# Performance work log

Hardware: AMD Instinct MI355X
Metric: run time of the kernel (lower is better)

Reference implementation:

```python
import jax, jax.numpy as jnp
import numpy as np

D_MODEL = 1024
N_HEADS = 16
HEAD_DIM = D_MODEL // N_HEADS


def _rotary_tables(seq_len, dim):
    # sin/cos tables: (seq_len, dim//2)
    pos = jnp.arange(seq_len, dtype=jnp.float32)[:, None]
    freqs = 1.0 / 10000.0 ** (jnp.arange(0, dim, 2, dtype=jnp.float32) / dim)
    angles = pos * freqs
    return jnp.sin(angles), jnp.cos(angles)


def _apply_rotary(x, sin, cos):
    # x: (B, H, N, head_dim); sin/cos: (N, head_dim//2) broadcast over B,H
    d_half = x.shape[-1] // 2
    x1, x2 = x[..., :d_half], x[..., d_half:]
    return jnp.concatenate([x1 * cos - x2 * sin, x1 * sin + x2 * cos], axis=-1)


def setup_inputs() -> dict:
    key = jax.random.key(0)
    k_x, k_q, k_k, k_v, k_o = jax.random.split(key, 5)
    B, N = 4, 2048
    scale = 1.0 / np.sqrt(D_MODEL)
    return {
        "x": jax.random.normal(k_x, (B, N, D_MODEL), dtype=jnp.float32),
        "Wq": jax.random.normal(k_q, (D_MODEL, D_MODEL), dtype=jnp.float32) * scale,
        "Wk": jax.random.normal(k_k, (D_MODEL, D_MODEL), dtype=jnp.float32) * scale,
        "Wv": jax.random.normal(k_v, (D_MODEL, D_MODEL), dtype=jnp.float32) * scale,
        "Wo": jax.random.normal(k_o, (D_MODEL, D_MODEL), dtype=jnp.float32) * scale,
    }


def reference(x, Wq, Wk, Wv, Wo):
    B, N, _ = x.shape
    # nn.Linear(d, d, bias=False): y = x @ W.T ; view+transpose -> (B, H, N, hd)
    def proj(W):
        return jnp.einsum('bnd,ed->bne', x, W).reshape(B, N, N_HEADS, HEAD_DIM).transpose(0, 2, 1, 3)

    Q, K, V = proj(Wq), proj(Wk), proj(Wv)
    sin, cos = _rotary_tables(N, HEAD_DIM)
    Q = _apply_rotary(Q, sin, cos)
    K = _apply_rotary(K, sin, cos)

    # SDPA (non-causal, dropout=0): softmax(Q K^T / sqrt(hd)) V
    scores = jnp.einsum('bhqd,bhkd->bhqk', Q, K) / jnp.sqrt(jnp.asarray(HEAD_DIM, x.dtype))
    attn = jax.nn.softmax(scores, axis=-1)
    out = jnp.einsum('bhqk,bhkd->bhqd', attn, V)  # (B, H, N, hd)
    out = out.transpose(0, 2, 1, 3).reshape(B, N, D_MODEL)
    return jnp.einsum('bnd,ed->bne', out, Wo)
```

## Files before the change

kernel.cpp:

```cpp
#include <hip/hip_runtime.h>
#include <stdint.h>

#define SEQ    2048
#define DMODEL 1024
#define NHEADS 16
#define HDIM   64
#define BATCH  4
#define MTOT   (BATCH*SEQ)

typedef __attribute__((ext_vector_type(8)))  short s16x8;
typedef __attribute__((ext_vector_type(4)))  short s16x4;
typedef __attribute__((ext_vector_type(4)))  float f32x4;
typedef __attribute__((ext_vector_type(16))) float f32x16;

#define OFF_SIN  ((size_t)0)
#define OFF_COS  ((size_t)262144)
#define OFF_XHI  ((size_t)524288)
#define OFF_WQH  ((size_t)34078720)
#define OFF_WKH  ((size_t)38273024)
#define OFF_WVH  ((size_t)42467328)
#define OFF_WOH  ((size_t)46661632)
#define OFF_QR   ((size_t)50855936)
#define OFF_KR   ((size_t)67633152)
#define OFF_VT   ((size_t)84410368)
#define OFF_AHI  ((size_t)101187584)

#define QSCALE 0.18033688011112042f

__device__ __forceinline__ uint16_t f2bf(float f){
  union{float f;uint32_t u;}v; v.f=f;
  uint32_t r=v.u+0x7fffu+((v.u>>16)&1u);
  return (uint16_t)(r>>16);
}
__device__ __forceinline__ float bf2f(uint16_t u){
  union{uint32_t u;float f;}v; v.u=((uint32_t)u)<<16; return v.f;
}

__device__ __forceinline__ void async16(void* lds, const void* g){
  __builtin_amdgcn_global_load_lds(
    (const __attribute__((address_space(1))) void*)g,
    (__attribute__((address_space(3))) void*)lds, 16, 0, 0);
}

__device__ __forceinline__ float fexp2(float x){
#if __has_builtin(__builtin_amdgcn_exp2f)
  return __builtin_amdgcn_exp2f(x);
#else
  float r; asm("v_exp_f32 %0, %1" : "=v"(r) : "v"(x)); return r;
#endif
}
__device__ __forceinline__ float frcp(float x){
#if __has_builtin(__builtin_amdgcn_rcpf)
  return __builtin_amdgcn_rcpf(x);
#else
  float r; asm("v_rcp_f32 %0, %1" : "=v"(r) : "v"(x)); return r;
#endif
}
__device__ __forceinline__ void plswap(unsigned a, unsigned b, unsigned &o0, unsigned &o1){
#if __has_builtin(__builtin_amdgcn_permlane32_swap)
  auto r = __builtin_amdgcn_permlane32_swap(a, b, false, false);
  o0 = (unsigned)r[0]; o1 = (unsigned)r[1];
#else
  unsigned ax = (unsigned)__shfl_xor((int)a, 32, 64);
  unsigned bx = (unsigned)__shfl_xor((int)b, 32, 64);
  bool hi = (threadIdx.x & 32) != 0;
  o0 = hi ? bx : a;
  o1 = hi ? b  : ax;
#endif
}

__global__ __launch_bounds__(256) void prep_k(
  const float* __restrict__ x,
  const float* __restrict__ Wq, const float* __restrict__ Wk,
  const float* __restrict__ Wv, const float* __restrict__ Wo,
  uint16_t* __restrict__ xhi, uint16_t* __restrict__ wqh, uint16_t* __restrict__ wkh,
  uint16_t* __restrict__ wvh, uint16_t* __restrict__ woh,
  float* __restrict__ st, float* __restrict__ ct)
{
  int b = blockIdx.x;
  if (b < 12288){
    const float* s; uint16_t* d; int i;
    if (b < 8192){ s = x; d = xhi; i = b*256 + threadIdx.x; }
    else {
      int wsel = (b - 8192) >> 10;
      int lb   = (b - 8192) & 1023;
      s = wsel==0? Wq : wsel==1? Wk : wsel==2? Wv : Wo;
      d = wsel==0? wqh: wsel==1? wkh: wsel==2? wvh: woh;
      i = lb*256 + threadIdx.x;
    }
    f32x4 v = *(const f32x4*)(s + (size_t)i*4);
    s16x4 vh;
    #pragma unroll
    for(int r=0;r<4;r++) vh[r] = (short)f2bf(v[r]);
    *(s16x4*)(d + (size_t)i*4) = vh;
  } else {
    int i = (b - 12288)*256 + threadIdx.x;
    int n = i>>5, j = i&31;
    double freq = pow(10000.0, -(double)j/32.0);
    double ang = (double)n*freq;
    st[i] = (float)sin(ang);
    ct[i] = (float)cos(ang);
  }
}

__device__ __forceinline__ void gemm_mainloop64(
  const uint16_t* __restrict__ A, const uint16_t* __restrict__ B,
  int m0, int e0, char* lA, char* lB, f32x4 acc[4][4])
{
  const int t = threadIdx.x;
  const int lane = t & 63;
  const int wr = t>>7, wc = (t>>6)&1;
  const int lq = lane&15, lg = lane>>4;
  const int rowA = wr*64 + lq;
  const int rowB = wc*64 + lq;

  int dbyte[4], srow[4], sbyte[4];
  #pragma unroll
  for (int s=0;s<4;s++){
    int d = s*4096 + t*16;
    int r = d>>7, c = (d>>4)&7;
    dbyte[s]=d; srow[s]=r; sbyte[s]=(c ^ (r&7))*16;
  }
  int chh[2];
  #pragma unroll
  for (int kh=0;kh<2;kh++) chh[kh] = (((kh<<2)|lg) ^ (lq&7))*16;

  const char* Ab = (const char*)A;
  const char* Bb = (const char*)B;

  for (int k0=0; k0<DMODEL; k0+=64){
    #pragma unroll
    for (int s=0;s<4;s++){
      async16(lA + dbyte[s], Ab + (size_t)(m0+srow[s])*2048 + k0*2 + sbyte[s]);
      async16(lB + dbyte[s], Bb + (size_t)(e0+srow[s])*2048 + k0*2 + sbyte[s]);
    }
    __syncthreads();
    #pragma unroll
    for (int kh=0;kh<2;kh++){
      s16x8 af[4], bfr[4];
      #pragma unroll
      for (int mi=0;mi<4;mi++) af[mi]  = *(const s16x8*)(lA + (rowA+mi*16)*128 + chh[kh]);
      #pragma unroll
      for (int ni=0;ni<4;ni++) bfr[ni] = *(const s16x8*)(lB + (rowB+ni*16)*128 + chh[kh]);
      __builtin_amdgcn_s_setprio(1);
      #pragma unroll
      for (int mi=0;mi<4;mi++){
        #pragma unroll
        for (int ni=0;ni<4;ni++)
          acc[mi][ni] = __builtin_amdgcn_mfma_f32_16x16x32_bf16(af[mi], bfr[ni], acc[mi][ni],0,0,0);
      }
      __builtin_amdgcn_s_setprio(0);
    }
    __syncthreads();
  }
}

__global__ __launch_bounds__(256) void gemm_qkv_k(
  const uint16_t* __restrict__ Xh,
  const uint16_t* __restrict__ WqH, const uint16_t* __restrict__ WkH, const uint16_t* __restrict__ WvH,
  const float* __restrict__ st, const float* __restrict__ ct,
  uint16_t* __restrict__ Qr, uint16_t* __restrict__ Kr, uint16_t* __restrict__ Vt)
{
  __shared__ char lA[128*128], lB[128*128];
  int m0 = blockIdx.x*128;
  int cti = blockIdx.y;
  int seg = cti>>3;
  int e0 = (cti&7)*128;
  const uint16_t* W = seg==0? WqH : (seg==1? WkH : WvH);
  f32x4 acc[4][4];
  #pragma unroll
  for(int i=0;i<4;i++){
    #pragma unroll
    for(int j=0;j<4;j++) acc[i][j] = (f32x4){0.f,0.f,0.f,0.f};
  }
  gemm_mainloop64(Xh, W, m0, e0, lA, lB, acc);

  int t=threadIdx.x, lane=t&63, lq=lane&15, lg=lane>>4;
  int wr=t>>7, wc=(t>>6)&1;
  int eb = e0 + wc*64;
  int h = eb>>6;
  int rbase = m0 + wr*64 + lg*4;
  if (seg<2){
    uint16_t* O = seg==0? Qr:Kr;
    float qs = seg==0 ? QSCALE : 1.0f;
    #pragma unroll
    for(int mi=0;mi<4;mi++){
      #pragma unroll
      for(int ni=0;ni<2;ni++){
        int j = ni*16+lq;
        #pragma unroll
        for(int r=0;r<4;r++){
          int m = rbase + mi*16 + r;
          int b = m>>11, n = m&2047;
          float sv = st[n*32+j], cv = ct[n*32+j];
          float x1 = acc[mi][ni][r], x2 = acc[mi][ni+2][r];
          size_t base = ((size_t)((b*NHEADS+h)*SEQ + n))*HDIM;
          O[base + j]      = f2bf((x1*cv - x2*sv)*qs);
          O[base + j + 32] = f2bf((x1*sv + x2*cv)*qs);
        }
      }
    }
  } else {
    #pragma unroll
    for(int mi=0;mi<4;mi++){
      #pragma unroll
      for(int ni=0;ni<4;ni++){
        int dh = ni*16+lq;
        int m = rbase + mi*16;
        int b = m>>11, n = m&2047;
        s16x4 v;
        #pragma unroll
        for(int r=0;r<4;r++) v[r] = (short)f2bf(acc[mi][ni][r]);
        *(s16x4*)(Vt + ((size_t)((b*NHEADS+h)*HDIM + dh))*SEQ + n) = v;
      }
    }
  }
}

__global__ __launch_bounds__(256) void attn_k(
  const uint16_t* __restrict__ Qr, const uint16_t* __restrict__ Kr, const uint16_t* __restrict__ Vt,
  uint16_t* __restrict__ Ah)
{
  __shared__ char lds[32768];

  int bid = blockIdx.x;
  int w = (bid & 7)*128 + (bid >> 3);
  int bh = w >> 4, qt = w & 15;
  int tid = threadIdx.x;
  int wid = tid >> 6, lane = tid & 63;
  int l31 = lane & 31, hi = lane >> 5;
  int q0 = qt*128 + wid*32;

  const uint16_t* Qb = Qr + (size_t)bh*SEQ*HDIM;
  const uint16_t* Kb = Kr + (size_t)bh*SEQ*HDIM;
  const uint16_t* Vb = Vt + (size_t)bh*HDIM*SEQ;

  s16x8 qf[4];
  #pragma unroll
  for (int sp=0; sp<4; ++sp)
    qf[sp] = *(const s16x8*)(Qb + (size_t)(q0 + l31)*HDIM + sp*16 + hi*8);

  s16x8 ones;
  #pragma unroll
  for (int j=0;j<8;j++) ones[j] = (short)0x3F80;

  f32x16 zm16;
  #pragma unroll
  for (int r=0;r<16;r++) zm16[r] = -16.0f;

  f32x16 oa[2], lacc;
  #pragma unroll
  for (int r=0;r<16;r++){ oa[0][r]=0.f; oa[1][r]=0.f; lacc[r]=0.f; }

  const int e7 = l31 & 7;
  const int rK = l31*128;
  const int kOff[4]  = { (((0+hi)^e7)<<4), (((2+hi)^e7)<<4), (((4+hi)^e7)<<4), (((6+hi)^e7)<<4) };
  const int vA0 = (((0+hi)^e7)<<4), vA1 = (((2+hi)^e7)<<4);
  const int vB0 = (((4+hi)^e7)<<4), vB1 = (((6+hi)^e7)<<4);
  const bool odd = (wid & 1) != 0;
  const int kBaseF = odd ? 4096 : 0,   kBaseS = odd ? 0 : 4096;
  const int vF0 = odd ? vB0 : vA0,     vF1 = odd ? vB1 : vA1;
  const int vS0 = odd ? vA0 : vB0,     vS1 = odd ? vA1 : vB1;

  auto STAGE = [&](int buf, int t){
    const char* Ks = (const char*)(Kb + (size_t)t*64*HDIM);
    char* dK = lds + buf*8192;
    char* dV = lds + 16384 + buf*8192;
    #pragma unroll
    for (int r=0; r<2; ++r){
      int ci = r*256 + tid;
      int sc = ci ^ ((ci>>3)&7);
      async16(dK + ci*16, Ks + sc*16);
    }
    #pragma unroll
    for (int r=0; r<2; ++r){
      int ci = r*256 + tid;
      int row = ci>>3;
      int sc = (ci&7) ^ (row&7);
      async16(dV + ci*16, (const char*)Vb + ((size_t)row*SEQ + (size_t)t*64)*2 + sc*16);
    }
  };

  auto SUBSTEP = [&](const char* bK, const char* bV, int kbase, int v0, int v1){
    s16x8 kf[4];
    #pragma unroll
    for (int sp=0; sp<4; ++sp)
      kf[sp] = *(const s16x8*)(bK + kbase + rK + kOff[sp]);
    f32x16 sacc = zm16;
    __builtin_amdgcn_s_setprio(1);
    #pragma unroll
    for (int sp=0; sp<4; ++sp)
      sacc = __builtin_amdgcn_mfma_f32_32x32x16_bf16(kf[sp], qf[sp], sacc, 0,0,0);
    __builtin_amdgcn_s_setprio(0);
    s16x8 vf[4];
    #pragma unroll
    for (int db=0; db<2; ++db){
      vf[db*2+0] = *(const s16x8*)(bV + db*4096 + rK + v0);
      vf[db*2+1] = *(const s16x8*)(bV + db*4096 + rK + v1);
    }
    float p[16];
    #pragma unroll
    for (int r=0;r<16;r++) p[r] = fexp2(sacc[r]);
    uint32_t pw[8];
    #pragma unroll
    for (int j=0;j<8;j++)
      asm("v_cvt_pk_bf16_f32 %0, %1, %2" : "=v"(pw[j]) : "v"(p[2*j]), "v"(p[2*j+1]));
    unsigned w0,w1,w2,w3, x0,x1,x2,x3;
    plswap(pw[0], pw[2], w0, w2);
    plswap(pw[1], pw[3], w1, w3);
    plswap(pw[4], pw[6], x0, x2);
    plswap(pw[5], pw[7], x1, x3);
    union { uint32_t wd[4]; s16x8 v; } pa0, pa1;
    pa0.wd[0]=w0; pa0.wd[1]=w1; pa0.wd[2]=w2; pa0.wd[3]=w3;
    pa1.wd[0]=x0; pa1.wd[1]=x1; pa1.wd[2]=x2; pa1.wd[3]=x3;
    __builtin_amdgcn_s_setprio(1);
    oa[0] = __builtin_amdgcn_mfma_f32_32x32x16_bf16(pa0.v, vf[0], oa[0], 0,0,0);
    oa[0] = __builtin_amdgcn_mfma_f32_32x32x16_bf16(pa1.v, vf[1], oa[0], 0,0,0);
    oa[1] = __builtin_amdgcn_mfma_f32_32x32x16_bf16(pa0.v, vf[2], oa[1], 0,0,0);
    oa[1] = __builtin_amdgcn_mfma_f32_32x32x16_bf16(pa1.v, vf[3], oa[1], 0,0,0);
    lacc = __builtin_amdgcn_mfma_f32_32x32x16_bf16(pa0.v, ones, lacc, 0,0,0);
    lacc = __builtin_amdgcn_mfma_f32_32x32x16_bf16(pa1.v, ones, lacc, 0,0,0);
    __builtin_amdgcn_s_setprio(0);
  };

  STAGE(0, 0);
  asm volatile("s_waitcnt vmcnt(0)" ::: "memory");
  __syncthreads();

  const int NT = SEQ/64;
  for (int t=0; t<NT; ++t){
    int cur = t & 1;
    if (t+1 < NT) STAGE(cur^1, t+1);
    const char* bK = lds + cur*8192;
    const char* bV = lds + 16384 + cur*8192;
    SUBSTEP(bK, bV, kBaseF, vF0, vF1);
    SUBSTEP(bK, bV, kBaseS, vS0, vS1);
    asm volatile("s_waitcnt vmcnt(0)" ::: "memory");
    __syncthreads();
  }

  int b = bh >> 4, h = bh & 15;
  #pragma unroll
  for (int r=0;r<16;r++){
    int q = (r&3) + 8*(r>>2) + 4*hi;
    float inv = frcp(lacc[r]);
    size_t mrow = ((size_t)(b*SEQ + q0 + q))*DMODEL + (size_t)h*HDIM + l31;
    #pragma unroll
    for (int db=0; db<2; ++db)
      Ah[mrow + db*32] = f2bf(oa[db][r]*inv);
  }
}

__global__ __launch_bounds__(256) void gemm_out_k(
  const uint16_t* __restrict__ Ahp, const uint16_t* __restrict__ WoH, float* __restrict__ C)
{
  __shared__ char lA[128*128], lB[128*128];
  int m0 = blockIdx.x*128;
  int e0 = blockIdx.y*128;
  f32x4 acc[4][4];
  #pragma unroll
  for(int i=0;i<4;i++){
    #pragma unroll
    for(int j=0;j<4;j++) acc[i][j] = (f32x4){0.f,0.f,0.f,0.f};
  }
  gemm_mainloop64(Ahp, WoH, m0, e0, lA, lB, acc);
  int t=threadIdx.x, lane=t&63, lq=lane&15, lg=lane>>4;
  int wr=t>>7, wc=(t>>6)&1;
  int rbase = m0 + wr*64 + lg*4;
  int cb = e0 + wc*64;
  #pragma unroll
  for(int mi=0;mi<4;mi++){
    #pragma unroll
    for(int ni=0;ni<4;ni++){
      #pragma unroll
      for(int r=0;r<4;r++)
        C[(size_t)(rbase+mi*16+r)*DMODEL + cb + ni*16 + lq] = acc[mi][ni][r];
    }
  }
}

extern "C" void kernel_launch(void* const* d_in, const int* in_sizes, int n_in,
                              void* d_out, int out_size, void* d_ws, size_t ws_size,
                              hipStream_t stream) {
  const float* x  = (const float*)d_in[0];
  const float* Wq = (const float*)d_in[1];
  const float* Wk = (const float*)d_in[2];
  const float* Wv = (const float*)d_in[3];
  const float* Wo = (const float*)d_in[4];
  float* out = (float*)d_out;
  char* ws = (char*)d_ws;

  float* sin_t = (float*)(ws + OFF_SIN);
  float* cos_t = (float*)(ws + OFF_COS);
  uint16_t* xhi = (uint16_t*)(ws + OFF_XHI);
  uint16_t* wqh = (uint16_t*)(ws + OFF_WQH);
  uint16_t* wkh = (uint16_t*)(ws + OFF_WKH);
  uint16_t* wvh = (uint16_t*)(ws + OFF_WVH);
  uint16_t* woh = (uint16_t*)(ws + OFF_WOH);
  uint16_t* Qr  = (uint16_t*)(ws + OFF_QR);
  uint16_t* Kr  = (uint16_t*)(ws + OFF_KR);
  uint16_t* Vt  = (uint16_t*)(ws + OFF_VT);
  uint16_t* ahi = (uint16_t*)(ws + OFF_AHI);

  prep_k<<<dim3(12544),dim3(256),0,stream>>>(x, Wq, Wk, Wv, Wo,
                                             xhi, wqh, wkh, wvh, woh, sin_t, cos_t);

  gemm_qkv_k<<<dim3(MTOT/128, 24),dim3(256),0,stream>>>(xhi, wqh, wkh, wvh,
                                                        sin_t, cos_t, Qr, Kr, Vt);
  attn_k<<<dim3(BATCH*NHEADS*(SEQ/128)),dim3(256),0,stream>>>(Qr, Kr, Vt, ahi);
  gemm_out_k<<<dim3(MTOT/128, 8),dim3(256),0,stream>>>(ahi, woh, out);
}
```

Baseline: 198.4 us.

## Triple-buffer K tiles in attention and swizzle GEMM row-block order

The attention kernel now keeps K in a three-slot LDS ring, loaded two tiles ahead, while V stays double-buffered. The per-iteration wait becomes a partial vmcnt wait followed by a raw s_barrier, so the prefetched K loads can stay in flight across iterations. Both GEMM kernels remap blockIdx.x so that consecutive workgroups take row blocks spread across the M dimension, likely to improve cache or XCD locality. This adds LDS usage (40KB per block), which may lower occupancy, and relies on the vmcnt counts matching the number of outstanding async loads exactly.

```diff
diff --git a/kernel.cpp b/kernel.cpp
--- a/kernel.cpp
+++ b/kernel.cpp
@@ -162,7 +162,8 @@
   uint16_t* __restrict__ Qr, uint16_t* __restrict__ Kr, uint16_t* __restrict__ Vt)
 {
   __shared__ char lA[128*128], lB[128*128];
-  int m0 = blockIdx.x*128;
+  int mx = blockIdx.x;
+  int m0 = (((mx & 7) << 3) | (mx >> 3)) * 128;
   int cti = blockIdx.y;
   int seg = cti>>3;
   int e0 = (cti&7)*128;
@@ -221,7 +222,7 @@
   const uint16_t* __restrict__ Qr, const uint16_t* __restrict__ Kr, const uint16_t* __restrict__ Vt,
   uint16_t* __restrict__ Ah)
 {
-  __shared__ char lds[32768];
+  __shared__ char lds[40960];
 
   int bid = blockIdx.x;
   int w = (bid & 7)*128 + (bid >> 3);
@@ -262,22 +263,24 @@
   const int vF0 = odd ? vB0 : vA0,     vF1 = odd ? vB1 : vA1;
   const int vS0 = odd ? vA0 : vB0,     vS1 = odd ? vA1 : vB1;
 
-  auto STAGE = [&](int buf, int t){
-    const char* Ks = (const char*)(Kb + (size_t)t*64*HDIM);
-    char* dK = lds + buf*8192;
-    char* dV = lds + 16384 + buf*8192;
-    #pragma unroll
-    for (int r=0; r<2; ++r){
-      int ci = r*256 + tid;
-      int sc = ci ^ ((ci>>3)&7);
-      async16(dK + ci*16, Ks + sc*16);
-    }
+  auto STAGE_V = [&](int buf, int t){
+    char* dV = lds + 24576 + buf*8192;
     #pragma unroll
     for (int r=0; r<2; ++r){
       int ci = r*256 + tid;
       int row = ci>>3;
       int sc = (ci&7) ^ (row&7);
       async16(dV + ci*16, (const char*)Vb + ((size_t)row*SEQ + (size_t)t*64)*2 + sc*16);
+    }
+  };
+  auto STAGE_K = [&](int buf, int t){
+    const char* Ks = (const char*)(Kb + (size_t)t*64*HDIM);
+    char* dK = lds + buf*8192;
+    #pragma unroll
+    for (int r=0; r<2; ++r){
+      int ci = r*256 + tid;
+      int sc = ci ^ ((ci>>3)&7);
+      async16(dK + ci*16, Ks + sc*16);
     }
   };
 
@@ -323,20 +326,28 @@
     __builtin_amdgcn_s_setprio(0);
   };
 
-  STAGE(0, 0);
-  asm volatile("s_waitcnt vmcnt(0)" ::: "memory");
+  STAGE_V(0, 0);
+  STAGE_K(0, 0);
+  STAGE_K(1, 1);
+  asm volatile("s_waitcnt vmcnt(2)" ::: "memory");
   __syncthreads();
 
   const int NT = SEQ/64;
+  int kcur = 0;
   for (int t=0; t<NT; ++t){
-    int cur = t & 1;
-    if (t+1 < NT) STAGE(cur^1, t+1);
-    const char* bK = lds + cur*8192;
-    const char* bV = lds + 16384 + cur*8192;
+    if (t+1 < NT) STAGE_V((t+1)&1, t+1);
+    if (t+2 < NT){
+      int k2 = kcur+2; if (k2>=3) k2-=3;
+      STAGE_K(k2, t+2);
+    }
+    const char* bK = lds + kcur*8192;
+    const char* bV = lds + 24576 + (t&1)*8192;
     SUBSTEP(bK, bV, kBaseF, vF0, vF1);
     SUBSTEP(bK, bV, kBaseS, vS0, vS1);
-    asm volatile("s_waitcnt vmcnt(0)" ::: "memory");
-    __syncthreads();
+    if (t+2 < NT)      asm volatile("s_waitcnt vmcnt(2)" ::: "memory");
+    else if (t+1 < NT) asm volatile("s_waitcnt vmcnt(0)" ::: "memory");
+    if (t+1 < NT)      asm volatile("s_barrier" ::: "memory");
+    kcur = kcur+1; if (kcur>=3) kcur-=3;
   }
 
   int b = bh >> 4, h = bh & 15;
@@ -355,7 +366,8 @@
   const uint16_t* __restrict__ Ahp, const uint16_t* __restrict__ WoH, float* __restrict__ C)
 {
   __shared__ char lA[128*128], lB[128*128];
-  int m0 = blockIdx.x*128;
+  int mx = blockIdx.x;
+  int m0 = (((mx & 7) << 3) | (mx >> 3)) * 128;
   int e0 = blockIdx.y*128;
   f32x4 acc[4][4];
   #pragma unroll
```

Result: no change. 197.8 us (-0.3%).
